# Kernel optimization log

Measured on AMD Instinct MI355X. Metric: run time of the kernel, lower is better.

The kernel has to match this reference:

```python
import jax, jax.numpy as jnp
import numpy as np

P_TOP = 0.1          # fraction of brightest pixels for atmosphere
LEC_K = 3            # local-extremum conv kernel size (w=3 in forward)
HID = 64             # hidden channels of stand-in Net


def _conv2d(x, w, pad):
    return jax.lax.conv_general_dilated(
        x, w, window_strides=(1, 1), padding=[(pad, pad), (pad, pad)],
        dimension_numbers=("NCHW", "OIHW", "NCHW"))


def _lec_weights(k, dtype):
    # LocalExtremumConv.init_weights: all +/-1/k^2 with +/-1 at the center
    base = jnp.full((1, 1, k, k), 1.0 / (k * k), dtype=dtype)
    base = base.at[0, 0, k // 2, k // 2].set(1.0)
    return -base, base  # (min_weights, max_weights)


def setup_inputs() -> dict:
    key = jax.random.key(0)
    ks = jax.random.split(key, 8)
    B, C, H, W = 8, 3, 512, 512
    x = jax.random.uniform(ks[0], (B, C, H, W), dtype=jnp.float32)
    s1 = 1.0 / np.sqrt(C * 9)
    s2 = 1.0 / np.sqrt(HID * 9)
    return {
        "x": x,
        "net_w1": jax.random.normal(ks[1], (HID, C, 3, 3), jnp.float32) * s1,
        "net_b1": jnp.zeros((HID,), jnp.float32),
        "net_w2": jax.random.normal(ks[2], (C, HID, 3, 3), jnp.float32) * s2,
        "net_b2": jnp.zeros((C,), jnp.float32),
        "color_w": jax.random.normal(ks[3], (3, 3), jnp.float32) * (1.0 / np.sqrt(3)),
        "color_b": jnp.zeros((3,), jnp.float32),
        "conv_w": jax.random.normal(ks[4], (4, 3, 1, 1), jnp.float32) * (1.0 / np.sqrt(3)),
        "conv_b": jnp.zeros((4,), jnp.float32),
    }


def reference(x, net_w1, net_b1, net_w2, net_b2, color_w, color_b, conv_w, conv_b):
    B, C, H, W = x.shape
    # --- stand-in Net: 3->64->3 conv enhancement, sigmoid output ---
    h = jax.nn.relu(_conv2d(x, net_w1, 1) + net_b1[None, :, None, None])
    img_high = jax.nn.sigmoid(_conv2d(h, net_w2, 1) + net_b2[None, :, None, None])
    # --- stand-in Color_pred: GAP -> linear -> sigmoid -> (B,3,1,1) gain ---
    color = jax.nn.sigmoid(x.mean(axis=(2, 3)) @ color_w.T + color_b)
    img_high = img_high * color[:, :, None, None]
    # --- 1x1 conv -> split K (1ch), Bias (3ch); residual correction ---
    feat = _conv2d(img_high, conv_w, 0) + conv_b[None, :, None, None]
    K, Bt = feat[:, 0:1], feat[:, 1:4]
    x_out = K * x - Bt + x
    # --- illumination channel: reflect pad + channel min/max + LEC convs ---
    pad = LEC_K // 2
    xp = jnp.pad(x_out, ((0, 0), (0, 0), (pad, pad), (pad, pad)), mode="reflect")
    x_max = xp.max(axis=1, keepdims=True)
    _, max_w = _lec_weights(LEC_K, x.dtype)
    bright = jax.nn.relu(_conv2d(x_max, max_w, 0))  # (B,1,H,W)
    # --- atmosphere: top-p% brightest pixels, gather + mean ---
    # NOTE: faithful to torch images.view(B,-1,C) on NCHW (layout-scrambled)
    flat_img = x_out.reshape(B, H * W, C)
    flat_bright = bright.reshape(B, H * W)
    num_pixels = int(P_TOP * H * W)
    _, idx = jax.lax.top_k(flat_bright, num_pixels)          # (B, num_pixels)
    picked = jnp.take_along_axis(flat_img, idx[:, :, None], axis=1)
    A = picked.mean(axis=1)                                   # (B, C)
    return (x_out, A)
```

## Files before the change

### kernel.cpp

```cpp
#include <hip/hip_runtime.h>
#include <hip/hip_bf16.h>

#define Hn 512
#define Wn 512
#define HWn (512 * 512)
#define KTOP 26214

#define HBS 70
#define HBROW (18 * HBS)

typedef __attribute__((ext_vector_type(8))) short frag_ab;
typedef __attribute__((ext_vector_type(4))) float frag_cd;

__device__ __forceinline__ float sigf(float z) { return 1.0f / (1.0f + __expf(-z)); }

__device__ __forceinline__ short f2bf(float f) {
  unsigned u = __float_as_uint(f);
  u += 0x7FFFu + ((u >> 16) & 1u);
  return (short)(u >> 16);
}

__device__ __forceinline__ unsigned aload(const unsigned* p) {
  return __hip_atomic_load(p, __ATOMIC_RELAXED, __HIP_MEMORY_SCOPE_AGENT);
}

__global__ __launch_bounds__(256) void k_means(
    const float* __restrict__ x, float* __restrict__ means, unsigned* __restrict__ doneCnt,
    const float* __restrict__ w1, const float* __restrict__ b1, const float* __restrict__ w2,
    const float* __restrict__ cw, const float* __restrict__ cb,
    short* __restrict__ w1A, short* __restrict__ w2A, int* __restrict__ kbTab,
    float* __restrict__ colorG)
{
  const int tid = threadIdx.x;
  __shared__ int lastS;
  const int lid = blockIdx.x;
  const int b = lid & 7;
  const int r8 = lid >> 3;
  const int c = r8 >> 5, slice = r8 & 31;
  const int bc = b * 3 + c;
  const float4* p = (const float4*)(x + bc * HWn + slice * 8192);
  float s = 0.f;
  for (int i = tid; i < 2048; i += 256) { float4 v = p[i]; s += v.x + v.y + v.z + v.w; }
  for (int off = 32; off > 0; off >>= 1) s += __shfl_down(s, off);
  if ((tid & 63) == 0) atomicAdd(&means[bc], s);
  __syncthreads();
  if (tid == 0) {
    unsigned tk = __hip_atomic_fetch_add(doneCnt, 1u, __ATOMIC_RELAXED, __HIP_MEMORY_SCOPE_AGENT);
    lastS = (tk == 767);
  }
  __syncthreads();
  if (!lastS) return;

  {
    int chunk = tid >> 6, lane = tid & 63;
    int m = lane & 15, q = lane >> 4;
    for (int j = 0; j < 8; ++j) {
      int k = q * 8 + j;
      float v = (k < 27) ? w1[(chunk * 16 + m) * 27 + k] : 0.f;
      w1A[tid * 8 + j] = f2bf(v);
    }
  }
  if (tid < 64) {
    int q = tid >> 4;
    for (int j = 0; j < 8; ++j) {
      int k = q * 8 + j;
      int kk = (k < 27) ? k : (k - 27);
      int ic = kk / 9; int r = kk - ic * 9;
      kbTab[tid * 8 + j] = (ic * 240 + (r / 3) * 20 + (r % 3)) * 2;
    }
  }
  for (int i = tid; i < 384; i += 256) {
    int step = i >> 6, lane = i & 63;
    int m = lane & 15, q = lane >> 4;
    int dx = step >> 1, half = step & 1;
    int dy = m / 3, oc = m - dy * 3;
    for (int j = 0; j < 8; ++j) {
      int ch = half * 32 + q * 8 + j;
      float v = (m < 9) ? w2[oc * 576 + ch * 9 + dy * 3 + dx] : 0.f;
      w2A[i * 8 + j] = f2bf(v);
    }
  }
  if (tid < 24) {
    int bb = tid / 3, oc = tid % 3;
    float z = cb[oc];
    for (int j = 0; j < 3; ++j)
      z += (atomicAdd(&means[bb * 3 + j], 0.f) * (1.0f / (float)HWn)) * cw[oc * 3 + j];
    colorG[tid] = sigf(z);
  }
}

__global__ __launch_bounds__(256, 6) void k_fused(
    const float* __restrict__ x, const float* __restrict__ b1,
    const float* __restrict__ b2, const float* __restrict__ convw, const float* __restrict__ convb,
    const short* __restrict__ w1Ag, const short* __restrict__ w2Ag,
    const int* __restrict__ kbTab,
    const float* __restrict__ colorG, float* __restrict__ out, float* __restrict__ Mb)
{
  __shared__ __align__(16) unsigned short xs[720];
  __shared__ __align__(16) unsigned short hb[180 * HBS];
  __shared__ float bs[64];
  __shared__ float b2s[3], colorS[3], cwS[12], cbS[4];

  const int tid = threadIdx.x;
  const int wid = tid >> 6, lane = tid & 63;
  const int n = lane & 15, q = lane >> 4;

  const int lid = blockIdx.x + (blockIdx.y << 5) + (blockIdx.z << 11);
  const int swz = ((lid & 7) << 11) | (lid >> 3);
  const int txi = swz & 31, tyi = (swz >> 5) & 63;
  const int tx0 = txi * 16, ty0 = tyi * 8;
  const int b = swz >> 11;
  const bool inter = (txi - 1u) < 30u && (tyi - 1u) < 62u;

  if (tid < 180) {
    int c = tid / 60, rem = tid - c * 60;
    int yy = rem / 5, xq = (rem - yy * 5) * 4;
    int gy = ty0 - 2 + yy, gx0 = tx0 - 2 + xq;
    const float* rp = x + (b * 3 + c) * HWn + (gy << 9) + gx0;
    float v0, v1, v2, v3;
    if (inter) {
      v0 = rp[0]; v1 = rp[1]; v2 = rp[2]; v3 = rp[3];
    } else {
      bool rowok = (unsigned)gy < 512u;
      v0 = (rowok && (unsigned)(gx0 + 0) < 512u) ? rp[0] : 0.f;
      v1 = (rowok && (unsigned)(gx0 + 1) < 512u) ? rp[1] : 0.f;
      v2 = (rowok && (unsigned)(gx0 + 2) < 512u) ? rp[2] : 0.f;
      v3 = (rowok && (unsigned)(gx0 + 3) < 512u) ? rp[3] : 0.f;
    }
    __hip_bfloat162 c01 = __float22bfloat162_rn(make_float2(v0, v1));
    __hip_bfloat162 c23 = __float22bfloat162_rn(make_float2(v2, v3));
    uint2 v2w; v2w.x = *(unsigned*)&c01; v2w.y = *(unsigned*)&c23;
    *(uint2*)(xs + c * 240 + yy * 20 + xq) = v2w;
  }
  if (tid < 64) bs[tid] = b1[tid];
  if (tid < 3)  b2s[tid] = b2[tid];
  if (tid < 3)  colorS[tid] = colorG[b * 3 + tid];
  if (tid < 12) cwS[tid] = convw[tid];
  if (tid < 4)  cbS[tid] = convb[tid];

  frag_ab w1f[4];
#pragma unroll
  for (int ck = 0; ck < 4; ++ck) w1f[ck] = *(const frag_ab*)(w1Ag + (ck * 64 + lane) * 8);

  int kb[8];
  {
    const int4* kp = (const int4*)(kbTab + lane * 8);
    int4 ka = kp[0], kc = kp[1];
    kb[0] = ka.x; kb[1] = ka.y; kb[2] = ka.z; kb[3] = ka.w;
    kb[4] = kc.x; kb[5] = kc.y; kb[6] = kc.z; kb[7] = kc.w;
  }
  __syncthreads();

  float biasr[4][4];
#pragma unroll
  for (int ck = 0; ck < 4; ++ck)
#pragma unroll
    for (int r = 0; r < 4; ++r) biasr[ck][r] = bs[ck * 16 + q * 4 + r];

  if (inter) {
    for (int g = wid; g < 12; g += 4) {
      int pt = g * 16 + n;
      int ptc = (pt < 180) ? pt : 179;
      int pty = (ptc * 3641) >> 16;
      int ptx = ptc - pty * 18;
      int baseB = (pty * 20 + ptx) * 2;
      frag_ab B;
#pragma unroll
      for (int j = 0; j < 8; ++j)
        B[j] = *(const short*)((const char*)xs + baseB + kb[j]);
#pragma unroll
      for (int ck = 0; ck < 4; ++ck) {
        frag_cd D = {biasr[ck][0], biasr[ck][1], biasr[ck][2], biasr[ck][3]};
        D = __builtin_amdgcn_mfma_f32_16x16x32_bf16(w1f[ck], B, D, 0, 0, 0);
        float2 p01 = make_float2(fmaxf(D[0], 0.f), fmaxf(D[1], 0.f));
        float2 p23 = make_float2(fmaxf(D[2], 0.f), fmaxf(D[3], 0.f));
        __hip_bfloat162 c01 = __float22bfloat162_rn(p01);
        __hip_bfloat162 c23 = __float22bfloat162_rn(p23);
        uint2 v2; v2.x = *(unsigned*)&c01; v2.y = *(unsigned*)&c23;
        *(uint2*)(hb + ptc * HBS + ck * 16 + q * 4) = v2;
      }
    }
  } else {
    for (int g = wid; g < 12; g += 4) {
      int pt = g * 16 + n;
      int ptc = (pt < 180) ? pt : 179;
      int pty = (ptc * 3641) >> 16;
      int ptx = ptc - pty * 18;
      int baseB = (pty * 20 + ptx) * 2;
      int gy = ty0 - 1 + pty, gx = tx0 - 1 + ptx;
      bool valid = (unsigned)gy < 512u && (unsigned)gx < 512u;
      frag_ab B;
#pragma unroll
      for (int j = 0; j < 8; ++j)
        B[j] = *(const short*)((const char*)xs + baseB + kb[j]);
#pragma unroll
      for (int ck = 0; ck < 4; ++ck) {
        frag_cd D = {biasr[ck][0], biasr[ck][1], biasr[ck][2], biasr[ck][3]};
        D = __builtin_amdgcn_mfma_f32_16x16x32_bf16(w1f[ck], B, D, 0, 0, 0);
        float2 p01 = make_float2(fmaxf(D[0], 0.f), fmaxf(D[1], 0.f));
        float2 p23 = make_float2(fmaxf(D[2], 0.f), fmaxf(D[3], 0.f));
        __hip_bfloat162 c01 = __float22bfloat162_rn(p01);
        __hip_bfloat162 c23 = __float22bfloat162_rn(p23);
        unsigned lo = valid ? *(unsigned*)&c01 : 0u;
        unsigned hi = valid ? *(unsigned*)&c23 : 0u;
        uint2 v2; v2.x = lo; v2.y = hi;
        *(uint2*)(hb + ptc * HBS + ck * 16 + q * 4) = v2;
      }
    }
  }

  frag_ab w2f[6];
#pragma unroll
  for (int i = 0; i < 6; ++i) w2f[i] = *(const frag_ab*)(w2Ag + (i * 64 + lane) * 8);
  __syncthreads();

  for (int r = wid; r < 10; r += 4) {
    frag_cd acc = {0.f, 0.f, 0.f, 0.f};
#pragma unroll
    for (int i = 0; i < 6; ++i) {
      int dx = i >> 1;
      int chb = (i & 1) * 64 + q * 16;
      frag_ab Bf = *(const frag_ab*)((const char*)hb + (r * 18 + n + dx) * (HBS * 2) + chb);
      acc = __builtin_amdgcn_mfma_f32_16x16x32_bf16(w2f[i], Bf, acc, 0, 0, 0);
    }
    float* dp = (float*)(hb + r * HBROW) + n * 10 + q * 4;
    if (q < 2) {
      *(float2*)dp = make_float2(acc[0], acc[1]);
      *(float2*)(dp + 2) = make_float2(acc[2], acc[3]);
    } else if (q == 2) {
      dp[0] = acc[0];
    }
  }
  __syncthreads();

  if (tid < 128) {
    int y = tid >> 4, xcol = tid & 15;
    float a0 = b2s[0], a1 = b2s[1], a2 = b2s[2];
#pragma unroll
    for (int dy = 0; dy < 3; ++dy) {
      const float* dp = (const float*)(hb + (y + dy) * HBROW) + xcol * 10 + dy * 3;
      a0 += dp[0]; a1 += dp[1]; a2 += dp[2];
    }
    float ih0 = colorS[0] * sigf(a0);
    float ih1 = colorS[1] * sigf(a1);
    float ih2 = colorS[2] * sigf(a2);
    float Kv = cwS[0] * ih0 + cwS[1]  * ih1 + cwS[2]  * ih2 + cbS[0];
    float f1 = cwS[3] * ih0 + cwS[4]  * ih1 + cwS[5]  * ih2 + cbS[1];
    float f2 = cwS[6] * ih0 + cwS[7]  * ih1 + cwS[8]  * ih2 + cbS[2];
    float f3 = cwS[9] * ih0 + cwS[10] * ih1 + cwS[11] * ih2 + cbS[3];
    float xc0 = __bfloat162float(*(const __hip_bfloat16*)&xs[0 * 240 + (y + 2) * 20 + (xcol + 2)]);
    float xc1 = __bfloat162float(*(const __hip_bfloat16*)&xs[1 * 240 + (y + 2) * 20 + (xcol + 2)]);
    float xc2 = __bfloat162float(*(const __hip_bfloat16*)&xs[2 * 240 + (y + 2) * 20 + (xcol + 2)]);
    int oi = ((ty0 + y) << 9) + (tx0 + xcol);
    float o0 = Kv * xc0 - f1 + xc0;
    float o1 = Kv * xc1 - f2 + xc1;
    float o2 = Kv * xc2 - f3 + xc2;
    out[(b * 3 + 0) * HWn + oi] = o0;
    out[(b * 3 + 1) * HWn + oi] = o1;
    out[(b * 3 + 2) * HWn + oi] = o2;
    Mb[b * HWn + oi] = fmaxf(fmaxf(o0, o1), o2);
  }
}

__device__ __forceinline__ void softBarrier(unsigned* ctr, unsigned target) {
  __syncthreads();
  if (threadIdx.x == 0) {
    __hip_atomic_fetch_add(ctr, 1u, __ATOMIC_RELAXED, __HIP_MEMORY_SCOPE_AGENT);
    while (__hip_atomic_load(ctr, __ATOMIC_RELAXED, __HIP_MEMORY_SCOPE_AGENT) < target)
      __builtin_amdgcn_s_sleep(2);
  }
  __syncthreads();
}

__device__ void sel256(const unsigned* __restrict__ h, unsigned kneed,
                       unsigned* sm, unsigned* oBin, unsigned* oAbove)
{
  const int t = threadIdx.x;
  sm[t] = aload(&h[t]);
  __syncthreads();
  for (int d = 1; d < 256; d <<= 1) {
    unsigned add = (t + d < 256) ? sm[t + d] : 0u;
    __syncthreads();
    sm[t] += add;
    __syncthreads();
  }
  unsigned mine = sm[t];
  unsigned nxt = (t < 255) ? sm[t + 1] : 0u;
  if (mine >= kneed && nxt < kneed) { *oBin = (unsigned)t; *oAbove = nxt; }
  __syncthreads();
}

__device__ void sel4096(const unsigned* __restrict__ h, unsigned kneed,
                        unsigned* sm, unsigned* oBin, unsigned* oAbove)
{
  const int t = threadIdx.x;
  unsigned loc[16]; unsigned sum = 0;
#pragma unroll
  for (int i = 0; i < 16; ++i) { loc[i] = aload(&h[t * 16 + i]); sum += loc[i]; }
  sm[t] = sum;
  __syncthreads();
  for (int d = 1; d < 256; d <<= 1) {
    unsigned add = (t + d < 256) ? sm[t + d] : 0u;
    __syncthreads();
    sm[t] += add;
    __syncthreads();
  }
  unsigned mine = sm[t];
  unsigned nxt = (t < 255) ? sm[t + 1] : 0u;
  if (mine >= kneed && nxt < kneed) {
    unsigned acc = nxt;
    for (int i = 15; i >= 0; --i) {
      unsigned c = loc[i];
      if (acc + c >= kneed) { *oBin = (unsigned)(t * 16 + i); *oAbove = acc; break; }
      acc += c;
    }
  }
  __syncthreads();
}

__global__ __launch_bounds__(256) void k_tail(
    const float* __restrict__ Mbuf, const float* __restrict__ outv,
    unsigned* __restrict__ h1, unsigned* __restrict__ h12,
    unsigned* __restrict__ eqTaken, float* __restrict__ Asum,
    unsigned* __restrict__ barCtr, unsigned* __restrict__ doneCnt, float* __restrict__ outA)
{
  __shared__ __align__(16) char smem[20640];
  __shared__ __align__(16) float brightS[4096];
  __shared__ unsigned sB1, sA1, sB2, sA2;
  __shared__ float red[4][3];
  __shared__ int lastA;

  float (*xm)[516] = (float (*)[516])smem;
  unsigned* hh = (unsigned*)smem;
  unsigned* sm = (unsigned*)(smem + 16384);

  const int tid = threadIdx.x;
  const int lid = blockIdx.x;
  const int swz = ((lid & 7) << 6) | (lid >> 3);
  const int b = swz >> 6, strip = swz & 63;
  const int y0 = strip * 8;
  const float* mp = Mbuf + b * HWn;
  const float* op = outv + b * 3 * HWn;
  unsigned* bar = barCtr + b * 48;

  for (int idx = tid; idx < 1280; idx += 256) {
    int r = idx >> 7, seg = idx & 127;
    int gy = y0 - 1 + r; gy = (gy < 0) ? -gy : (gy > 511 ? 1022 - gy : gy);
    int c0 = seg * 4;
    float4 v = *(const float4*)(mp + (gy << 9) + c0);
    xm[r][c0 + 1] = v.x;
    xm[r][c0 + 2] = v.y;
    xm[r][c0 + 3] = v.z;
    xm[r][c0 + 4] = v.w;
  }
  if (tid < 20) {
    int r = tid >> 1, side = tid & 1;
    int gy = y0 - 1 + r; gy = (gy < 0) ? -gy : (gy > 511 ? 1022 - gy : gy);
    int gx = side ? 510 : 1;
    xm[r][side ? 513 : 0] = mp[(gy << 9) + gx];
  }
  __syncthreads();
  {
    const int row = tid >> 5, cl = tid & 31;
#pragma unroll 4
    for (int i = 0; i < 16; ++i) {
      int c = cl + (i << 5);
      float s0 = xm[row][c]     + xm[row][c + 1]     + xm[row][c + 2];
      float s1 = xm[row + 1][c] + xm[row + 1][c + 1] + xm[row + 1][c + 2];
      float s2 = xm[row + 2][c] + xm[row + 2][c + 1] + xm[row + 2][c + 2];
      float s = (s0 + s1 + s2) * (1.f / 9.f) + xm[row + 1][c + 1] * (8.f / 9.f);
      s = fmaxf(s, 0.f);
      brightS[(row << 9) + c] = s;
    }
  }
  __syncthreads();

  hh[tid] = 0;
  __syncthreads();
  {
    unsigned cb0 = 0x100, cc0 = 0, cb1 = 0x100, cc1 = 0;
    const float4* bp4 = (const float4*)brightS;
#pragma unroll
    for (int it = 0; it < 4; ++it) {
      float4 v = bp4[it * 256 + tid];
      unsigned bins[4] = { __float_as_uint(v.x) >> 24, __float_as_uint(v.y) >> 24,
                           __float_as_uint(v.z) >> 24, __float_as_uint(v.w) >> 24 };
#pragma unroll
      for (int j = 0; j < 4; ++j) {
        unsigned bb = bins[j];
        if (bb == cb0) ++cc0;
        else if (bb == cb1) ++cc1;
        else if (!cc0) { cb0 = bb; cc0 = 1; }
        else if (!cc1) { cb1 = bb; cc1 = 1; }
        else atomicAdd(&hh[bb], 1u);
      }
    }
    if (cc0) atomicAdd(&hh[cb0], cc0);
    if (cc1) atomicAdd(&hh[cb1], cc1);
  }
  __syncthreads();
  if (hh[tid]) atomicAdd(&h1[(b << 8) + tid], hh[tid]);
  softBarrier(bar, 64);

  sel256(h1 + (b << 8), KTOP, sm, &sB1, &sA1);
  for (int i = tid; i < 4096; i += 256) hh[i] = 0;
  __syncthreads();
  const float4* bp = (const float4*)brightS;
  const unsigned sb1 = sB1;
#pragma unroll
  for (int it = 0; it < 4; ++it) {
    float4 v = bp[it * 256 + tid];
    unsigned u0 = __float_as_uint(v.x), u1 = __float_as_uint(v.y);
    unsigned u2 = __float_as_uint(v.z), u3 = __float_as_uint(v.w);
    if ((u0 >> 24) == sb1) atomicAdd(&hh[(u0 >> 12) & 0xFFFu], 1u);
    if ((u1 >> 24) == sb1) atomicAdd(&hh[(u1 >> 12) & 0xFFFu], 1u);
    if ((u2 >> 24) == sb1) atomicAdd(&hh[(u2 >> 12) & 0xFFFu], 1u);
    if ((u3 >> 24) == sb1) atomicAdd(&hh[(u3 >> 12) & 0xFFFu], 1u);
  }
  __syncthreads();
  for (int i = tid; i < 4096; i += 256)
    if (hh[i]) atomicAdd(&h12[(b << 12) + i], hh[i]);
  if (tid == 0) { sB2 = 0xFFFu; sA2 = 0u; }
  softBarrier(bar + 16, 64);

  sel4096(h12 + (b << 12), KTOP - sA1, sm, &sB2, &sA2);
  const unsigned T20 = (sB1 << 12) | sB2;
  const unsigned ne = KTOP - sA1 - sA2;
  float v0 = 0.f, v1 = 0.f, v2 = 0.f;
  for (int it = 0; it < 16; ++it) {
    int li = it * 256 + tid;
    int pix = (y0 << 9) + li;
    unsigned u20 = __float_as_uint(brightS[li]) >> 12;
    bool take = u20 > T20;
    if (u20 == T20) {
      if (aload(&eqTaken[b * 16]) < ne) {
        unsigned old = atomicAdd(&eqTaken[b * 16], 1u);
        take = old < ne;
      }
    }
    if (take) {
      v0 += op[3 * pix];
      v1 += op[3 * pix + 1];
      v2 += op[3 * pix + 2];
    }
  }
  for (int off = 32; off > 0; off >>= 1) {
    v0 += __shfl_down(v0, off);
    v1 += __shfl_down(v1, off);
    v2 += __shfl_down(v2, off);
  }
  int w = tid >> 6;
  if ((tid & 63) == 0) { red[w][0] = v0; red[w][1] = v1; red[w][2] = v2; }
  __syncthreads();
  if (tid == 0) {
    atomicAdd(&Asum[b * 3 + 0], red[0][0] + red[1][0] + red[2][0] + red[3][0]);
    atomicAdd(&Asum[b * 3 + 1], red[0][1] + red[1][1] + red[2][1] + red[3][1]);
    atomicAdd(&Asum[b * 3 + 2], red[0][2] + red[1][2] + red[2][2] + red[3][2]);
  }
  __syncthreads();
  if (tid == 0) {
    unsigned tk = __hip_atomic_fetch_add(doneCnt, 1u, __ATOMIC_RELAXED, __HIP_MEMORY_SCOPE_AGENT);
    lastA = (tk == 511);
  }
  __syncthreads();
  if (lastA && tid < 24)
    outA[3 * HWn * 8 + tid] = atomicAdd(&Asum[tid], 0.f) * (1.0f / (float)KTOP);
}

extern "C" void kernel_launch(void* const* d_in, const int* in_sizes, int n_in,
                              void* d_out, int out_size, void* d_ws, size_t ws_size,
                              hipStream_t stream)
{
  const float* x     = (const float*)d_in[0];
  const float* w1    = (const float*)d_in[1];
  const float* b1    = (const float*)d_in[2];
  const float* w2    = (const float*)d_in[3];
  const float* b2    = (const float*)d_in[4];
  const float* cw    = (const float*)d_in[5];
  const float* cb    = (const float*)d_in[6];
  const float* convw = (const float*)d_in[7];
  const float* convb = (const float*)d_in[8];
  float* out = (float*)d_out;
  char* ws = (char*)d_ws;

  float*    Mbuf      = (float*)(ws);
  unsigned* h1        = (unsigned*)(ws + 8388608);
  unsigned* h12       = (unsigned*)(ws + 8396800);
  float*    Asum      = (float*)(ws + 8658944);
  unsigned* eqTaken   = (unsigned*)(ws + 8659040);
  float*    means     = (float*)(ws + 8659552);
  unsigned* meansDone = (unsigned*)(ws + 8659648);
  unsigned* accumDone = (unsigned*)(ws + 8659680);
  unsigned* barCtr    = (unsigned*)(ws + 8659712);
  short*    w1Ag      = (short*)(ws + 8661248);
  short*    w2Ag      = (short*)(ws + 8665344);
  float*    colorG    = (float*)(ws + 8683776);
  int*      kbTab     = (int*)(ws + 8683904);

  hipMemsetAsync(ws + 8388608, 0, 8661248 - 8388608, stream);

  k_means<<<768, 256, 0, stream>>>(x, means, meansDone, w1, b1, w2, cw, cb, w1Ag, w2Ag, kbTab, colorG);
  k_fused<<<dim3(32, 64, 8), 256, 0, stream>>>(x, b1, b2, convw, convb, w1Ag, w2Ag, kbTab, colorG, out, Mbuf);
  k_tail<<<512, 256, 0, stream>>>(Mbuf, out, h1, h12, eqTaken, Asum, barCtr, accumDone, out);
}
```

Baseline: 239.7 us.

## Fuse conv1 and conv2 per row to drop inter-stage block barrier

```diff
diff --git a/kernel.cpp b/kernel.cpp
--- a/kernel.cpp
+++ b/kernel.cpp
@@ -89,7 +89,7 @@
   }
 }
 
-__global__ __launch_bounds__(256, 6) void k_fused(
+__global__ __launch_bounds__(256, 5) void k_fused(
     const float* __restrict__ x, const float* __restrict__ b1,
     const float* __restrict__ b2, const float* __restrict__ convw, const float* __restrict__ convb,
     const short* __restrict__ w1Ag, const short* __restrict__ w2Ag,
@@ -141,6 +141,9 @@
   frag_ab w1f[4];
 #pragma unroll
   for (int ck = 0; ck < 4; ++ck) w1f[ck] = *(const frag_ab*)(w1Ag + (ck * 64 + lane) * 8);
+  frag_ab w2f[6];
+#pragma unroll
+  for (int i = 0; i < 6; ++i) w2f[i] = *(const frag_ab*)(w2Ag + (i * 64 + lane) * 8);
 
   int kb[8];
   {
@@ -157,38 +160,12 @@
 #pragma unroll
     for (int r = 0; r < 4; ++r) biasr[ck][r] = bs[ck * 16 + q * 4 + r];
 
-  if (inter) {
-    for (int g = wid; g < 12; g += 4) {
-      int pt = g * 16 + n;
-      int ptc = (pt < 180) ? pt : 179;
-      int pty = (ptc * 3641) >> 16;
-      int ptx = ptc - pty * 18;
-      int baseB = (pty * 20 + ptx) * 2;
-      frag_ab B;
-#pragma unroll
-      for (int j = 0; j < 8; ++j)
-        B[j] = *(const short*)((const char*)xs + baseB + kb[j]);
-#pragma unroll
-      for (int ck = 0; ck < 4; ++ck) {
-        frag_cd D = {biasr[ck][0], biasr[ck][1], biasr[ck][2], biasr[ck][3]};
-        D = __builtin_amdgcn_mfma_f32_16x16x32_bf16(w1f[ck], B, D, 0, 0, 0);
-        float2 p01 = make_float2(fmaxf(D[0], 0.f), fmaxf(D[1], 0.f));
-        float2 p23 = make_float2(fmaxf(D[2], 0.f), fmaxf(D[3], 0.f));
-        __hip_bfloat162 c01 = __float22bfloat162_rn(p01);
-        __hip_bfloat162 c23 = __float22bfloat162_rn(p23);
-        uint2 v2; v2.x = *(unsigned*)&c01; v2.y = *(unsigned*)&c23;
-        *(uint2*)(hb + ptc * HBS + ck * 16 + q * 4) = v2;
-      }
-    }
-  } else {
-    for (int g = wid; g < 12; g += 4) {
-      int pt = g * 16 + n;
-      int ptc = (pt < 180) ? pt : 179;
-      int pty = (ptc * 3641) >> 16;
-      int ptx = ptc - pty * 18;
-      int baseB = (pty * 20 + ptx) * 2;
-      int gy = ty0 - 1 + pty, gx = tx0 - 1 + ptx;
-      bool valid = (unsigned)gy < 512u && (unsigned)gx < 512u;
+  for (int r = wid; r < 10; r += 4) {
+    const int gyr = ty0 - 1 + r;
+    {
+      int baseB = (r * 20 + n) * 2;
+      bool valid = true;
+      if (!inter) valid = ((unsigned)gyr < 512u) && ((unsigned)(tx0 - 1 + n) < 512u);
       frag_ab B;
 #pragma unroll
       for (int j = 0; j < 8; ++j)
@@ -204,17 +181,34 @@
         unsigned lo = valid ? *(unsigned*)&c01 : 0u;
         unsigned hi = valid ? *(unsigned*)&c23 : 0u;
         uint2 v2; v2.x = lo; v2.y = hi;
-        *(uint2*)(hb + ptc * HBS + ck * 16 + q * 4) = v2;
+        *(uint2*)(hb + (r * 18 + n) * HBS + ck * 16 + q * 4) = v2;
       }
     }
-  }
-
-  frag_ab w2f[6];
-#pragma unroll
-  for (int i = 0; i < 6; ++i) w2f[i] = *(const frag_ab*)(w2Ag + (i * 64 + lane) * 8);
-  __syncthreads();
-
-  for (int r = wid; r < 10; r += 4) {
+    {
+      int col = (n < 2) ? (16 + n) : 17;
+      int baseB = (r * 20 + col) * 2;
+      bool valid = true;
+      if (!inter) valid = ((unsigned)gyr < 512u) && ((unsigned)(tx0 - 1 + col) < 512u);
+      frag_ab B;
+#pragma unroll
+      for (int j = 0; j < 8; ++j)
+        B[j] = *(const short*)((const char*)xs + baseB + kb[j]);
+#pragma unroll
+      for (int ck = 0; ck < 4; ++ck) {
+        frag_cd D = {biasr[ck][0], biasr[ck][1], biasr[ck][2], biasr[ck][3]};
+        D = __builtin_amdgcn_mfma_f32_16x16x32_bf16(w1f[ck], B, D, 0, 0, 0);
+        float2 p01 = make_float2(fmaxf(D[0], 0.f), fmaxf(D[1], 0.f));
+        float2 p23 = make_float2(fmaxf(D[2], 0.f), fmaxf(D[3], 0.f));
+        __hip_bfloat162 c01 = __float22bfloat162_rn(p01);
+        __hip_bfloat162 c23 = __float22bfloat162_rn(p23);
+        unsigned lo = valid ? *(unsigned*)&c01 : 0u;
+        unsigned hi = valid ? *(unsigned*)&c23 : 0u;
+        if (n < 2) {
+          uint2 v2; v2.x = lo; v2.y = hi;
+          *(uint2*)(hb + (r * 18 + col) * HBS + ck * 16 + q * 4) = v2;
+        }
+      }
+    }
     frag_cd acc = {0.f, 0.f, 0.f, 0.f};
 #pragma unroll
     for (int i = 0; i < 6; ++i) {
```

Result: slower. 258.2 us (+7.7%).
